# Optimization experiments

Measured on AMD Instinct MI355X. Metric: run time of the kernel, lower is better.

Reference implementation:

```python
import jax, jax.numpy as jnp
import numpy as np

GROUP_SIZE = 64  # int4 precision
QMAX = 7.0       # symmetric int4 quant scale divisor


def setup_inputs() -> dict:
    key = jax.random.key(0)
    ks = jax.random.split(key, 8)
    B, S, C_in, C_out, R = 1, 4096, 3072, 3072, 32
    G = C_in // GROUP_SIZE
    x = jax.random.normal(ks[0], (B, S, C_in), dtype=jnp.float32)
    # unpacked int4 weight codes in [0,16); reference subtracts 8 -> signed int4 [-8,7]
    qweight = jax.random.randint(ks[1], (C_out, C_in), 0, 16, dtype=jnp.int32)
    # small positive per-group, per-out-channel weight scales
    wscales = jax.random.uniform(ks[2], (G, C_out), dtype=jnp.float32) * 0.01 + 0.001
    # positive smoothing factors bounded away from zero
    smooth_factor = jax.random.uniform(ks[3], (C_in,), dtype=jnp.float32) + 0.5
    proj_down = jax.random.normal(ks[4], (C_in, R), dtype=jnp.float32) * (1.0 / np.sqrt(C_in))
    proj_up = jax.random.normal(ks[5], (C_out, R), dtype=jnp.float32) * (1.0 / np.sqrt(R))
    bias = jax.random.normal(ks[6], (C_out,), dtype=jnp.float32) * 0.02
    return {
        "x": x,
        "qweight": qweight,
        "wscales": wscales,
        "smooth_factor": smooth_factor,
        "proj_down": proj_down,
        "proj_up": proj_up,
        "bias": bias,
    }


def reference(x, qweight, wscales, smooth_factor, proj_down, proj_up, bias):
    B, S, C = x.shape
    C_out = qweight.shape[0]
    M = B * S
    G = C // GROUP_SIZE

    # --- smoothing: x_hat = x / s (SVDQuant smoothing on activations) ---
    xs = x.reshape(M, C) / smooth_factor  # (M, C)

    # --- low-rank branch hidden state (fused with quantization in CUDA kernel) ---
    lora_act = jnp.einsum('mc,cr->mr', xs, proj_down)  # (M, R)

    # --- dynamic per-token, per-group int4 activation quantization ---
    xg = xs.reshape(M, G, GROUP_SIZE)
    amax = jnp.max(jnp.abs(xg), axis=-1, keepdims=True)          # (M, G, 1)
    ascale = amax / QMAX
    q = jnp.clip(jnp.round(xg / jnp.maximum(ascale, 1e-8)), -8.0, 7.0)
    x_dq = (q * ascale).reshape(M, C)                            # dequantized activations

    # --- weight dequantization: signed int4 codes * per-group/out-channel scales ---
    qw = qweight.astype(jnp.float32) - 8.0                       # (C_out, C) in [-8, 7]
    w_dq = (qw.reshape(C_out, G, GROUP_SIZE) * wscales.T[:, :, None]).reshape(C_out, C)

    # --- quantized GEMM + low-rank correction + bias ---
    out = jnp.einsum('mc,oc->mo', x_dq, w_dq)
    out = out + jnp.einsum('mr,or->mo', lora_act, proj_up) + bias
    return out.reshape(B, S, C_out)
```

## Files before the change

kernel.cpp:

```cpp
#include <hip/hip_runtime.h>
#include <stdint.h>

typedef unsigned short u16;

#define MTOK 4096
#define CIN  3072
#define COUT 3072
#define RANK 32
#define RS   3136
#define LKSPLIT 16
#define LKC (CIN/LKSPLIT)
#define WROWS 6

typedef __attribute__((ext_vector_type(8))) short bf16x8;
typedef __attribute__((ext_vector_type(4))) float f32x4;

__device__ __forceinline__ u16 f2bf(float f) {
  union { float f; unsigned u; } v; v.f = f;
  unsigned r = v.u + 0x7FFFu + ((v.u >> 16) & 1u);
  return (u16)(r >> 16);
}

__device__ __forceinline__ void gload_lds16(const void* g, void* l) {
  __builtin_amdgcn_global_load_lds(
      (const __attribute__((address_space(1))) unsigned int*)g,
      (__attribute__((address_space(3))) unsigned int*)l, 16, 0, 0);
}

__device__ __forceinline__ float quant1(float xs, float ascale, float qd) {
  float q = rintf(xs / qd);
  q = fminf(fmaxf(q, -8.f), 7.f);
  return q * ascale;
}

__global__ __launch_bounds__(256) void prep_kernel(
    const float* __restrict__ x, const float* __restrict__ smooth,
    const int* __restrict__ qw, const float* __restrict__ wsc,
    const float* __restrict__ pd, const float* __restrict__ pu,
    u16* __restrict__ xdq, u16* __restrict__ wdq, u16* __restrict__ pu_bf,
    float* __restrict__ lp)
{
  const int b = blockIdx.x;
  const int t = threadIdx.x;

#pragma unroll
  for (int r = 0; r < WROWS; ++r) {
    const int o = b * WROWS + r;
    const int4* qrow = (const int4*)(qw + (size_t)o * CIN);
    u16* orow = wdq + (size_t)o * RS;
#pragma unroll
    for (int p = 0; p < 3; ++p) {
      const int c4 = p * 256 + t;
      const int g = (c4 * 4) >> 6;
      const float ws = wsc[g * COUT + o];
      const int4 qv = qrow[c4];
      ushort4 ov;
      ov.x = f2bf((float)(qv.x - 8) * ws);
      ov.y = f2bf((float)(qv.y - 8) * ws);
      ov.z = f2bf((float)(qv.z - 8) * ws);
      ov.w = f2bf((float)(qv.w - 8) * ws);
      ((ushort4*)orow)[c4] = ov;
    }
  }
  if (t < WROWS * RANK) {
    const int o = b * WROWS + (t >> 5);
    pu_bf[(size_t)o * RANK + (t & 31)] = f2bf(pu[(size_t)o * RANK + (t & 31)]);
  }

  __shared__ __align__(16) u16 sA[128 * 64];
  __shared__ __align__(16) u16 sB[32 * 64];
  const int m0 = (b >> 4) * 128;
  const int kblk = b & 15;
  const int wave = t >> 6, lane = t & 63;
  const int lm = lane & 15, lkq = (lane >> 4) * 8;

  f32x4 acc[2][2];
  const f32x4 fz = {0.f, 0.f, 0.f, 0.f};
#pragma unroll
  for (int i = 0; i < 2; ++i)
#pragma unroll
    for (int j = 0; j < 2; ++j) acc[i][j] = fz;

  for (int kt = 0; kt < LKC / 64; ++kt) {
    const int k0 = kblk * LKC + kt * 64;
    const int col = (t & 15) * 4;
#pragma unroll
    for (int it = 0; it < 8; ++it) {
      const int row = it * 16 + (t >> 4);
      const float4 xv = *(const float4*)(x + (size_t)(m0 + row) * CIN + k0 + col);
      const float4 sv = *(const float4*)(smooth + k0 + col);
      const float xs0 = xv.x / sv.x, xs1 = xv.y / sv.y;
      const float xs2 = xv.z / sv.z, xs3 = xv.w / sv.w;
      ushort4 ov;
      ov.x = f2bf(xs0); ov.y = f2bf(xs1); ov.z = f2bf(xs2); ov.w = f2bf(xs3);
      *(ushort4*)&sA[row * 64 + col] = ov;
      float a = fmaxf(fmaxf(fabsf(xs0), fabsf(xs1)), fmaxf(fabsf(xs2), fabsf(xs3)));
#pragma unroll
      for (int off = 1; off < 16; off <<= 1) a = fmaxf(a, __shfl_xor(a, off));
      const float ascale = a / 7.0f;
      const float qd = fmaxf(ascale, 1e-8f);
      ushort4 oq;
      oq.x = f2bf(quant1(xs0, ascale, qd));
      oq.y = f2bf(quant1(xs1, ascale, qd));
      oq.z = f2bf(quant1(xs2, ascale, qd));
      oq.w = f2bf(quant1(xs3, ascale, qd));
      *(ushort4*)(xdq + (size_t)(m0 + row) * RS + k0 + col) = oq;
    }
#pragma unroll
    for (int i = 0; i < 8; ++i) {
      const int idx = i * 256 + t;
      const int k = idx >> 5, r = idx & 31;
      sB[r * 64 + k] = f2bf(pd[(size_t)(k0 + k) * RANK + r]);
    }
    __syncthreads();
#pragma unroll
    for (int kk = 0; kk < 2; ++kk) {
      const int ko = kk * 32 + lkq;
      bf16x8 af[2], bfr[2];
#pragma unroll
      for (int i = 0; i < 2; ++i)
        af[i] = *(const bf16x8*)&sA[(wave * 32 + i * 16 + lm) * 64 + ko];
#pragma unroll
      for (int j = 0; j < 2; ++j)
        bfr[j] = *(const bf16x8*)&sB[(j * 16 + lm) * 64 + ko];
#pragma unroll
      for (int i = 0; i < 2; ++i)
#pragma unroll
        for (int j = 0; j < 2; ++j)
          acc[i][j] = __builtin_amdgcn_mfma_f32_16x16x32_bf16(af[i], bfr[j], acc[i][j], 0, 0, 0);
    }
    __syncthreads();
  }
  float* lpk = lp + (size_t)kblk * MTOK * RANK;
#pragma unroll
  for (int i = 0; i < 2; ++i)
#pragma unroll
    for (int j = 0; j < 2; ++j) {
      const int col = j * 16 + lm;
      const int row0 = m0 + wave * 32 + i * 16 + (lane >> 4) * 4;
#pragma unroll
      for (int r = 0; r < 4; ++r)
        lpk[(size_t)(row0 + r) * RANK + col] = acc[i][j][r];
    }
}

__global__ __launch_bounds__(256) void lora_fix_kernel(
    const float* __restrict__ lp, u16* __restrict__ lora_bf)
{
  const int idx = blockIdx.x * 256 + threadIdx.x;
  const int m = idx >> 5, c = idx & 31;
  float s = 0.f;
#pragma unroll
  for (int k = 0; k < LKSPLIT; ++k) s += lp[((size_t)k * MTOK + m) * RANK + c];
  lora_bf[(size_t)m * RANK + c] = f2bf(s);
}


__device__ __forceinline__ void stage_half(const u16* __restrict__ g, u16* lds_base,
                                           int kt, int half, int buf, int t) {
#pragma unroll
  for (int r = 0; r < 2; ++r) {
    const int ld = r * 512 + t;
    const int row = ld >> 3;
    const int d = ld & 7;
    const int c16 = d ^ (row & 7);
    gload_lds16(g + (size_t)(half * 128 + row) * RS + kt * 64 + c16 * 8,
                lds_base + buf * 16384 + half * 8192 + ld * 8);
  }
}

#define DSA(buf, mh) \
  _Pragma("unroll") for (int i = 0; i < 4; ++i) { \
    const int rl = wm * 64 + i * 16 + lm; \
    _Pragma("unroll") for (int kk = 0; kk < 2; ++kk) \
      af[i][kk] = *(const bf16x8*)&lds[(buf)*16384 + (mh)*8192 + rl * 64 + \
                    ((((kk << 2) | q4) ^ (rl & 7)) << 3)]; \
  }

#define DSB(buf, nh, BF) \
  _Pragma("unroll") for (int j = 0; j < 2; ++j) { \
    const int rl = wn * 32 + j * 16 + lm; \
    _Pragma("unroll") for (int kk = 0; kk < 2; ++kk) \
      BF[j][kk] = *(const bf16x8*)&lds[32768 + (buf)*16384 + (nh)*8192 + rl * 64 + \
                    ((((kk << 2) | q4) ^ (rl & 7)) << 3)]; \
  }

#define MFMA_Q(mh, nh, BF) \
  __builtin_amdgcn_s_setprio(1); \
  _Pragma("unroll") for (int i = 0; i < 4; ++i) \
  _Pragma("unroll") for (int j = 0; j < 2; ++j) \
  _Pragma("unroll") for (int kk = 0; kk < 2; ++kk) \
    acc[(mh)*4 + i][(nh)*2 + j] = __builtin_amdgcn_mfma_f32_16x16x32_bf16( \
        af[i][kk], BF[j][kk], acc[(mh)*4 + i][(nh)*2 + j], 0, 0, 0); \
  __builtin_amdgcn_s_setprio(0);

#define PH_OPEN() \
  __builtin_amdgcn_sched_barrier(0); \
  __builtin_amdgcn_s_barrier(); \
  asm volatile("s_waitcnt lgkmcnt(0)" ::: "memory"); \
  __builtin_amdgcn_sched_barrier(0)

#define PH_CLOSE() \
  __builtin_amdgcn_sched_barrier(0); \
  __builtin_amdgcn_s_barrier(); \
  __builtin_amdgcn_sched_barrier(0)

#define VM8() asm volatile("s_waitcnt vmcnt(8)" ::: "memory")
#define VM0() asm volatile("s_waitcnt vmcnt(0)" ::: "memory")

#define TILE8(cur, S_A0, S_B0, S_B1, S_A1, VMI) do { \
  DSA(cur, 0); DSB(cur, 0, bf0); \
  PH_OPEN(); MFMA_Q(0, 0, bf0); PH_CLOSE(); \
  DSB(cur, 1, bf1); S_A0; S_B0; \
  PH_OPEN(); MFMA_Q(0, 1, bf1); PH_CLOSE(); \
  DSA(cur, 1); S_B1; \
  PH_OPEN(); MFMA_Q(1, 1, bf1); PH_CLOSE(); \
  S_A1; \
  PH_OPEN(); MFMA_Q(1, 0, bf0); VMI; PH_CLOSE(); \
} while (0)

__global__ __launch_bounds__(512, 2) void gemm_kernel(
    const u16* __restrict__ xdq, const u16* __restrict__ wdq,
    const u16* __restrict__ pu_bf, const u16* __restrict__ lora_bf,
    const float* __restrict__ bias, float* __restrict__ out)
{
  __shared__ __align__(16) u16 lds[65536];

  const int t = threadIdx.x;
  const int wid = t >> 6, lane = t & 63;
  const int wm = wid >> 2, wn = wid & 3;
  const int lm = lane & 15, q4 = lane >> 4;

  const int wg = blockIdx.x;
  const int swz = (wg & 7) * 24 + (wg >> 3);
  const int by = swz / 12, bx = swz % 12;
  const int m0 = by * 256, n0 = bx * 256;

  const u16* Ag = xdq + (size_t)m0 * RS;
  const u16* Bg = wdq + (size_t)n0 * RS;
  u16* ldsB = lds + 32768;

  f32x4 acc[8][4];
  const f32x4 fz = {0.f, 0.f, 0.f, 0.f};
#pragma unroll
  for (int i = 0; i < 8; ++i)
#pragma unroll
    for (int j = 0; j < 4; ++j) acc[i][j] = fz;

  bf16x8 af[4][2], bf0[2][2], bf1[2][2];

  stage_half(Ag, lds,  0, 0, 0, t);
  stage_half(Bg, ldsB, 0, 0, 0, t);
  stage_half(Bg, ldsB, 0, 1, 0, t);
  stage_half(Ag, lds,  0, 1, 0, t);
  stage_half(Ag, lds,  1, 0, 1, t);
  stage_half(Bg, ldsB, 1, 0, 1, t);
  stage_half(Bg, ldsB, 1, 1, 1, t);
  stage_half(Ag, lds,  1, 1, 1, t);
  VM8();
  __builtin_amdgcn_s_barrier();
  __builtin_amdgcn_sched_barrier(0);

  for (int T = 0; T < 46; T += 2) {
    TILE8(0,
          stage_half(Ag, lds,  T + 2, 0, 0, t),
          stage_half(Bg, ldsB, T + 2, 0, 0, t),
          stage_half(Bg, ldsB, T + 2, 1, 0, t),
          stage_half(Ag, lds,  T + 2, 1, 0, t),
          VM8());
    TILE8(1,
          stage_half(Ag, lds,  T + 3, 0, 1, t),
          stage_half(Bg, ldsB, T + 3, 0, 1, t),
          stage_half(Bg, ldsB, T + 3, 1, 1, t),
          stage_half(Ag, lds,  T + 3, 1, 1, t),
          VM8());
  }
  TILE8(0, (void)0, (void)0, (void)0, (void)0, VM0());
  TILE8(1, (void)0, (void)0, (void)0, (void)0, (void)0);

  bf16x8 bl[4];
#pragma unroll
  for (int b = 0; b < 4; ++b) {
    const int bcol = n0 + (b >> 1) * 128 + wn * 32 + (b & 1) * 16 + lm;
    bl[b] = *(const bf16x8*)(pu_bf + (size_t)bcol * RANK + q4 * 8);
  }
#pragma unroll
  for (int a = 0; a < 8; ++a) {
    const int arow = m0 + (a >> 2) * 128 + wm * 64 + (a & 3) * 16 + lm;
    const bf16x8 al = *(const bf16x8*)(lora_bf + (size_t)arow * RANK + q4 * 8);
#pragma unroll
    for (int b = 0; b < 4; ++b)
      acc[a][b] = __builtin_amdgcn_mfma_f32_16x16x32_bf16(al, bl[b], acc[a][b], 0, 0, 0);
  }

#pragma unroll
  for (int b = 0; b < 4; ++b) {
    const int col = n0 + (b >> 1) * 128 + wn * 32 + (b & 1) * 16 + lm;
    const float bv = bias[col];
#pragma unroll
    for (int a = 0; a < 8; ++a) {
      const int row0 = m0 + (a >> 2) * 128 + wm * 64 + (a & 3) * 16 + q4 * 4;
#pragma unroll
      for (int r = 0; r < 4; ++r)
        out[(size_t)(row0 + r) * COUT + col] = acc[a][b][r] + bv;
    }
  }
}

extern "C" void kernel_launch(void* const* d_in, const int* in_sizes, int n_in,
                              void* d_out, int out_size, void* d_ws, size_t ws_size,
                              hipStream_t stream) {
  const float* x      = (const float*)d_in[0];
  const int*   qw     = (const int*)d_in[1];
  const float* wsc    = (const float*)d_in[2];
  const float* smooth = (const float*)d_in[3];
  const float* pd     = (const float*)d_in[4];
  const float* pu     = (const float*)d_in[5];
  const float* bias   = (const float*)d_in[6];
  float* out = (float*)d_out;

  u16* xdq     = (u16*)d_ws;
  u16* wdq     = xdq + (size_t)MTOK * RS;
  u16* pu_bf   = wdq + (size_t)COUT * RS;
  u16* lora_bf = pu_bf + (size_t)COUT * RANK;
  float* lp    = (float*)(lora_bf + (size_t)MTOK * RANK);

  prep_kernel<<<512, 256, 0, stream>>>(
      x, smooth, qw, wsc, pd, pu, xdq, wdq, pu_bf, lp);
  lora_fix_kernel<<<MTOK * RANK / 256, 256, 0, stream>>>(lp, lora_bf);
  gemm_kernel<<<192, 512, 0, stream>>>(
      xdq, wdq, pu_bf, lora_bf, bias, out);
}
```

Measured before the change: 229.7 us.

## Retile GEMM to 256x192 blocks so grid fills all 256 CUs

Changes the GEMM workgroup tile from 256x256 to 256x192, producing 256 workgroups instead of 192 so each CU gets one tile. Wave layout changes to 4x2 with 32x96 sub-tiles, B staging is rewritten for 192-row tiles with uneven load distribution, and LDS shrinks. The goal is removing wave-quantization idle CUs, at the cost of lower per-tile reuse and more redundant A loads.

Result: faster. 218.3 us (-4.9%).

```diff
diff --git a/kernel.cpp b/kernel.cpp
--- a/kernel.cpp
+++ b/kernel.cpp
@@ -156,42 +156,59 @@
 }
 
 
-__device__ __forceinline__ void stage_half(const u16* __restrict__ g, u16* lds_base,
-                                           int kt, int half, int buf, int t) {
+__device__ __forceinline__ void stage_A_half(const u16* __restrict__ g, u16* lds0,
+                                             int kt, int half, int buf, int t) {
 #pragma unroll
   for (int r = 0; r < 2; ++r) {
-    const int ld = r * 512 + t;
-    const int row = ld >> 3;
-    const int d = ld & 7;
-    const int c16 = d ^ (row & 7);
+    const int id = r * 512 + t;
+    const int row = id >> 3;
+    const int sl = id & 7;
+    const int c16 = sl ^ (row & 7);
     gload_lds16(g + (size_t)(half * 128 + row) * RS + kt * 64 + c16 * 8,
-                lds_base + buf * 16384 + half * 8192 + ld * 8);
+                lds0 + buf * 16384 + half * 8192 + id * 8);
+  }
+}
+
+__device__ __forceinline__ void stage_B_half(const u16* __restrict__ g, u16* lds0,
+                                             int kt, int nh, int buf, int t) {
+  u16* base = lds0 + 32768 + buf * 12288 + nh * 6144;
+  {
+    const int row = t >> 3, sl = t & 7;
+    const int c16 = sl ^ (row & 7);
+    gload_lds16(g + (size_t)(nh * 96 + row) * RS + kt * 64 + c16 * 8, base + t * 8);
+  }
+  if (nh ? (t >= 256) : (t < 256)) {
+    const int et = t - (nh ? 256 : 0);
+    const int row = 64 + (et >> 3), sl = et & 7;
+    const int c16 = sl ^ (row & 7);
+    gload_lds16(g + (size_t)(nh * 96 + row) * RS + kt * 64 + c16 * 8,
+                base + 4096 + et * 8);
   }
 }
 
 #define DSA(buf, mh) \
-  _Pragma("unroll") for (int i = 0; i < 4; ++i) { \
-    const int rl = wm * 64 + i * 16 + lm; \
+  _Pragma("unroll") for (int i_ = 0; i_ < 2; ++i_) { \
+    const int rl = wm * 32 + i_ * 16 + lm; \
     _Pragma("unroll") for (int kk = 0; kk < 2; ++kk) \
-      af[i][kk] = *(const bf16x8*)&lds[(buf)*16384 + (mh)*8192 + rl * 64 + \
+      af[i_][kk] = *(const bf16x8*)&lds[(buf)*16384 + (mh)*8192 + rl * 64 + \
                     ((((kk << 2) | q4) ^ (rl & 7)) << 3)]; \
   }
 
-#define DSB(buf, nh, BF) \
-  _Pragma("unroll") for (int j = 0; j < 2; ++j) { \
-    const int rl = wn * 32 + j * 16 + lm; \
+#define DSB(buf, nh, BQ) \
+  _Pragma("unroll") for (int j_ = 0; j_ < 3; ++j_) { \
+    const int rb = wn * 48 + j_ * 16 + lm; \
     _Pragma("unroll") for (int kk = 0; kk < 2; ++kk) \
-      BF[j][kk] = *(const bf16x8*)&lds[32768 + (buf)*16384 + (nh)*8192 + rl * 64 + \
-                    ((((kk << 2) | q4) ^ (rl & 7)) << 3)]; \
-  }
-
-#define MFMA_Q(mh, nh, BF) \
+      BQ[j_][kk] = *(const bf16x8*)&lds[32768 + (buf)*12288 + (nh)*6144 + rb * 64 + \
+                    ((((kk << 2) | q4) ^ (rb & 7)) << 3)]; \
+  }
+
+#define MFMA_Q(mh, nh, BQ) \
   __builtin_amdgcn_s_setprio(1); \
-  _Pragma("unroll") for (int i = 0; i < 4; ++i) \
-  _Pragma("unroll") for (int j = 0; j < 2; ++j) \
+  _Pragma("unroll") for (int i_ = 0; i_ < 2; ++i_) \
+  _Pragma("unroll") for (int j_ = 0; j_ < 3; ++j_) \
   _Pragma("unroll") for (int kk = 0; kk < 2; ++kk) \
-    acc[(mh)*4 + i][(nh)*2 + j] = __builtin_amdgcn_mfma_f32_16x16x32_bf16( \
-        af[i][kk], BF[j][kk], acc[(mh)*4 + i][(nh)*2 + j], 0, 0, 0); \
+    acc[(mh)*2 + i_][(nh)*3 + j_] = __builtin_amdgcn_mfma_f32_16x16x32_bf16( \
+        af[i_][kk], BQ[j_][kk], acc[(mh)*2 + i_][(nh)*3 + j_], 0, 0, 0); \
   __builtin_amdgcn_s_setprio(0);
 
 #define PH_OPEN() \
@@ -205,18 +222,18 @@
   __builtin_amdgcn_s_barrier(); \
   __builtin_amdgcn_sched_barrier(0)
 
-#define VM8() asm volatile("s_waitcnt vmcnt(8)" ::: "memory")
+#define VM7() asm volatile("s_waitcnt vmcnt(7)" ::: "memory")
 #define VM0() asm volatile("s_waitcnt vmcnt(0)" ::: "memory")
 
-#define TILE8(cur, S_A0, S_B0, S_B1, S_A1, VMI) do { \
-  DSA(cur, 0); DSB(cur, 0, bf0); \
-  PH_OPEN(); MFMA_Q(0, 0, bf0); PH_CLOSE(); \
-  DSB(cur, 1, bf1); S_A0; S_B0; \
-  PH_OPEN(); MFMA_Q(0, 1, bf1); PH_CLOSE(); \
+#define TILE4(cur, S_A0, S_B0, S_B1, S_A1, VMI) do { \
+  DSA(cur, 0); DSB(cur, 0, bq0); \
+  PH_OPEN(); MFMA_Q(0, 0, bq0); PH_CLOSE(); \
+  DSB(cur, 1, bq1); S_A0; S_B0; \
+  PH_OPEN(); MFMA_Q(0, 1, bq1); PH_CLOSE(); \
   DSA(cur, 1); S_B1; \
-  PH_OPEN(); MFMA_Q(1, 1, bf1); PH_CLOSE(); \
+  PH_OPEN(); MFMA_Q(1, 1, bq1); PH_CLOSE(); \
   S_A1; \
-  PH_OPEN(); MFMA_Q(1, 0, bf0); VMI; PH_CLOSE(); \
+  PH_OPEN(); MFMA_Q(1, 0, bq0); VMI; PH_CLOSE(); \
 } while (0)
 
 __global__ __launch_bounds__(512, 2) void gemm_kernel(
@@ -224,82 +241,81 @@
     const u16* __restrict__ pu_bf, const u16* __restrict__ lora_bf,
     const float* __restrict__ bias, float* __restrict__ out)
 {
-  __shared__ __align__(16) u16 lds[65536];
+  __shared__ __align__(16) u16 lds[57344];
 
   const int t = threadIdx.x;
   const int wid = t >> 6, lane = t & 63;
-  const int wm = wid >> 2, wn = wid & 3;
+  const int wm = wid >> 1, wn = wid & 1;
   const int lm = lane & 15, q4 = lane >> 4;
 
   const int wg = blockIdx.x;
-  const int swz = (wg & 7) * 24 + (wg >> 3);
-  const int by = swz / 12, bx = swz % 12;
-  const int m0 = by * 256, n0 = bx * 256;
+  const int swz = (wg & 7) * 32 + (wg >> 3);
+  const int by = swz >> 4, bx = swz & 15;
+  const int m0 = by * 256, n0 = bx * 192;
 
   const u16* Ag = xdq + (size_t)m0 * RS;
   const u16* Bg = wdq + (size_t)n0 * RS;
-  u16* ldsB = lds + 32768;
-
-  f32x4 acc[8][4];
+
+  f32x4 acc[4][6];
   const f32x4 fz = {0.f, 0.f, 0.f, 0.f};
 #pragma unroll
-  for (int i = 0; i < 8; ++i)
-#pragma unroll
-    for (int j = 0; j < 4; ++j) acc[i][j] = fz;
-
-  bf16x8 af[4][2], bf0[2][2], bf1[2][2];
-
-  stage_half(Ag, lds,  0, 0, 0, t);
-  stage_half(Bg, ldsB, 0, 0, 0, t);
-  stage_half(Bg, ldsB, 0, 1, 0, t);
-  stage_half(Ag, lds,  0, 1, 0, t);
-  stage_half(Ag, lds,  1, 0, 1, t);
-  stage_half(Bg, ldsB, 1, 0, 1, t);
-  stage_half(Bg, ldsB, 1, 1, 1, t);
-  stage_half(Ag, lds,  1, 1, 1, t);
-  VM8();
+  for (int i = 0; i < 4; ++i)
+#pragma unroll
+    for (int j = 0; j < 6; ++j) acc[i][j] = fz;
+
+  bf16x8 af[2][2], bq0[3][2], bq1[3][2];
+
+  stage_A_half(Ag, lds, 0, 0, 0, t);
+  stage_B_half(Bg, lds, 0, 0, 0, t);
+  stage_B_half(Bg, lds, 0, 1, 0, t);
+  stage_A_half(Ag, lds, 0, 1, 0, t);
+  stage_A_half(Ag, lds, 1, 0, 1, t);
+  stage_B_half(Bg, lds, 1, 0, 1, t);
+  stage_B_half(Bg, lds, 1, 1, 1, t);
+  stage_A_half(Ag, lds, 1, 1, 1, t);
+  VM7();
   __builtin_amdgcn_s_barrier();
   __builtin_amdgcn_sched_barrier(0);
 
   for (int T = 0; T < 46; T += 2) {
-    TILE8(0,
-          stage_half(Ag, lds,  T + 2, 0, 0, t),
-          stage_half(Bg, ldsB, T + 2, 0, 0, t),
-          stage_half(Bg, ldsB, T + 2, 1, 0, t),
-          stage_half(Ag, lds,  T + 2, 1, 0, t),
-          VM8());
-    TILE8(1,
-          stage_half(Ag, lds,  T + 3, 0, 1, t),
-          stage_half(Bg, ldsB, T + 3, 0, 1, t),
-          stage_half(Bg, ldsB, T + 3, 1, 1, t),
-          stage_half(Ag, lds,  T + 3, 1, 1, t),
-          VM8());
-  }
-  TILE8(0, (void)0, (void)0, (void)0, (void)0, VM0());
-  TILE8(1, (void)0, (void)0, (void)0, (void)0, (void)0);
-
-  bf16x8 bl[4];
-#pragma unroll
-  for (int b = 0; b < 4; ++b) {
-    const int bcol = n0 + (b >> 1) * 128 + wn * 32 + (b & 1) * 16 + lm;
+    TILE4(0,
+          stage_A_half(Ag, lds, T + 2, 0, 0, t),
+          stage_B_half(Bg, lds, T + 2, 0, 0, t),
+          stage_B_half(Bg, lds, T + 2, 1, 0, t),
+          stage_A_half(Ag, lds, T + 2, 1, 0, t),
+          VM7());
+    TILE4(1,
+          stage_A_half(Ag, lds, T + 3, 0, 1, t),
+          stage_B_half(Bg, lds, T + 3, 0, 1, t),
+          stage_B_half(Bg, lds, T + 3, 1, 1, t),
+          stage_A_half(Ag, lds, T + 3, 1, 1, t),
+          VM7());
+  }
+  TILE4(0, (void)0, (void)0, (void)0, (void)0, VM0());
+  TILE4(1, (void)0, (void)0, (void)0, (void)0, (void)0);
+
+  bf16x8 bl[6];
+#pragma unroll
+  for (int b = 0; b < 6; ++b) {
+    const int bcol = n0 + (b / 3) * 96 + wn * 48 + (b % 3) * 16 + lm;
     bl[b] = *(const bf16x8*)(pu_bf + (size_t)bcol * RANK + q4 * 8);
   }
 #pragma unroll
-  for (int a = 0; a < 8; ++a) {
-    const int arow = m0 + (a >> 2) * 128 + wm * 64 + (a & 3) * 16 + lm;
+  for (int a = 0; a < 4; ++a) {
+    const int arow = m0 + (a >> 1) * 128 + wm * 32 + (a & 1) * 16 + lm;
     const bf16x8 al = *(const bf16x8*)(lora_bf + (size_t)arow * RANK + q4 * 8);
 #pragma unroll
-    for (int b = 0; b < 4; ++b)
+    for (int b = 0; b < 6; ++b)
       acc[a][b] = __builtin_amdgcn_mfma_f32_16x16x32_bf16(al, bl[b], acc[a][b], 0, 0, 0);
   }
 
 #pragma unroll
-  for (int b = 0; b < 4; ++b) {
-    const int col = n0 + (b >> 1) * 128 + wn * 32 + (b & 1) * 16 + lm;
+  for (int b = 0; b < 6; ++b) {
+    const int col = n0 + (b / 3) * 96 + wn * 48 + (b % 3) * 16 + lm;
     const float bv = bias[col];
 #pragma unroll
-    for (int a = 0; a < 8; ++a) {
-      const int row0 = m0 + (a >> 2) * 128 + wm * 64 + (a & 3) * 16 + q4 * 4;
+    for (int a = 0; a < 4; ++a) {
+      const int row0 = m0 + (a >> 1) * 128 + wm * 32 + (a & 1) * 16 + q4 * 4;
 #pragma unroll
       for (int r = 0; r < 4; ++r)
         out[(size_t)(row0 + r) * COUT + col] = acc[a][b][r] + bv;
@@ -328,6 +344,6 @@
   prep_kernel<<<512, 256, 0, stream>>>(
       x, smooth, qw, wsc, pd, pu, xdq, wdq, pu_bf, lp);
   lora_fix_kernel<<<MTOK * RANK / 256, 256, 0, stream>>>(lp, lora_bf);
-  gemm_kernel<<<192, 512, 0, stream>>>(
+  gemm_kernel<<<256, 512, 0, stream>>>(
       xdq, wdq, pu_bf, lora_bf, bias, out);
 }
```
